# Optimization experiments

Measured on AMD Instinct MI355X. Metric: run time of the kernel, lower is better.

## Reference

```python
import jax, jax.numpy as jnp
import numpy as np

N_NODES = 100000
N_EDGES = 1600000
D_IN = 128
D_HID = 128


def setup_inputs() -> dict:
    key = jax.random.key(0)
    ks = jax.random.split(key, 7)
    s_in = 1.0 / np.sqrt(D_IN)
    s_hid = 1.0 / np.sqrt(D_HID)
    return {
        "x": jax.random.normal(ks[0], (N_NODES, D_IN), dtype=jnp.float32),
        "edge_index": jax.random.randint(ks[1], (2, N_EDGES), 0, N_NODES, dtype=jnp.int64),
        "W1_l": jax.random.normal(ks[2], (D_IN, D_HID), dtype=jnp.float32) * s_in,
        "b1": jnp.zeros((D_HID,), dtype=jnp.float32),
        "W1_r": jax.random.normal(ks[3], (D_IN, D_HID), dtype=jnp.float32) * s_in,
        "W2_l": jax.random.normal(ks[4], (D_HID, D_HID), dtype=jnp.float32) * s_hid,
        "b2": jnp.zeros((D_HID,), dtype=jnp.float32),
        "W2_r": jax.random.normal(ks[5], (D_HID, D_HID), dtype=jnp.float32) * s_hid,
    }


def _mean_aggregate(x, src, dst, num_nodes):
    # messages x[src] mean-aggregated at dst (PyG SAGEConv default aggr='mean')
    msg = jnp.take(x, src, axis=0)                       # [E, D] gather
    summed = jax.ops.segment_sum(msg, dst, num_segments=num_nodes)  # [N, D]
    deg = jax.ops.segment_sum(jnp.ones((src.shape[0],), x.dtype), dst,
                              num_segments=num_nodes)
    return summed / jnp.maximum(deg, 1.0)[:, None]


def _sage_conv(x, src, dst, W_l, b, W_r):
    agg = _mean_aggregate(x, src, dst, x.shape[0])
    # out = lin_l(aggregated neighbors) + lin_r(root)
    return agg @ W_l + b + x @ W_r


def reference(x, edge_index, W1_l, b1, W1_r, W2_l, b2, W2_r):
    src, dst = edge_index[0], edge_index[1]
    h = _sage_conv(x, src, dst, W1_l, b1, W1_r)
    h = jax.nn.relu(h)  # dropout inactive in eval mode
    out = _sage_conv(h, src, dst, W2_l, b2, W2_r)
    return out
```

## Files before the change

kernel.cpp:

```cpp
#include <hip/hip_runtime.h>

#define NN 100000
#define NE 1600000
#define DF 128
#define NBUCK 391
#define PA_BLOCKS 784
#define PB_BLOCKS 391
#define CX_BLOCKS 3125
#define CW_BLOCKS 64
#define AGG_GRID 3128

typedef short short8 __attribute__((ext_vector_type(8)));
typedef float floatx4 __attribute__((ext_vector_type(4)));
typedef float floatx2 __attribute__((ext_vector_type(2)));
typedef unsigned int uintx4 __attribute__((ext_vector_type(4)));
typedef unsigned int uint;
typedef unsigned short ushort;
typedef unsigned char uchar;

static __device__ __forceinline__ ushort f2bf(float f) {
    uint u = __builtin_bit_cast(uint, f);
    return (ushort)((u + 0x7fffu + ((u >> 16) & 1u)) >> 16);
}

__global__ __launch_bounds__(256) void pA_hist(const int* __restrict__ dst,
                                               int* __restrict__ hist,
                                               ushort* __restrict__ rank8) {
    __shared__ int h[NBUCK];
    int tid = threadIdx.x;
    for (int i = tid; i < NBUCK; i += 256) h[i] = 0;
    __syncthreads();
    int eb = blockIdx.x * 2048 + tid;
    #pragma unroll
    for (int k = 0; k < 8; ++k) {
        int e = eb + k * 256;
        if (e < NE) {
            int r = atomicAdd(&h[dst[e] >> 8], 1);
            rank8[e] = (ushort)r;
        }
    }
    __syncthreads();
    int* hrow = hist + blockIdx.x * NBUCK;
    for (int i = tid; i < NBUCK; i += 256) hrow[i] = h[i];
}

__global__ __launch_bounds__(256) void pS2_colscan(int* __restrict__ hist,
                                                   int* __restrict__ gt) {
    __shared__ int ps[256];
    int b = blockIdx.x;
    int tid = threadIdx.x;
    int v[4];
    int sum = 0;
    #pragma unroll
    for (int k = 0; k < 4; ++k) {
        int blk = tid * 4 + k;
        v[k] = (blk < PA_BLOCKS) ? hist[blk * NBUCK + b] : 0;
        sum += v[k];
    }
    ps[tid] = sum;
    __syncthreads();
    for (int st = 1; st < 256; st <<= 1) {
        int t = (tid >= st) ? ps[tid - st] : 0;
        __syncthreads();
        ps[tid] += t;
        __syncthreads();
    }
    int excl = ps[tid] - sum;
    #pragma unroll
    for (int k = 0; k < 4; ++k) {
        int blk = tid * 4 + k;
        if (blk < PA_BLOCKS) hist[blk * NBUCK + b] = excl;
        excl += v[k];
    }
    if (tid == 255) gt[b] = excl;
}

__global__ __launch_bounds__(512) void pS_scan(const int* __restrict__ gt,
                                               int* __restrict__ goff) {
    __shared__ int s[512];
    int tid = threadIdx.x;
    int v = (tid < NBUCK) ? gt[tid] : 0;
    s[tid] = v;
    __syncthreads();
    for (int st = 1; st < 512; st <<= 1) {
        int t = (tid >= st) ? s[tid - st] : 0;
        __syncthreads();
        s[tid] += t;
        __syncthreads();
    }
    if (tid < NBUCK) goff[tid] = s[tid] - v;
    if (tid == 0) goff[NBUCK] = NE;
}

__global__ __launch_bounds__(512) void fused_mid(
        const int* __restrict__ src, const int* __restrict__ dst,
        const ushort* __restrict__ rank8, const int* __restrict__ rel,
        const int* __restrict__ goff, uint2* __restrict__ pairs,
        const float* __restrict__ x, ushort* __restrict__ xb, uint* __restrict__ xf8,
        const float* __restrict__ W1l, const float* __restrict__ W1r,
        const float* __restrict__ W2l, const float* __restrict__ W2r,
        ushort* __restrict__ WT1, ushort* __restrict__ WT2) {
    int bid = blockIdx.x;
    int tid = threadIdx.x;
    if (bid < PB_BLOCKS) {
        int eb = bid * 4096 + tid;
        #pragma unroll
        for (int k = 0; k < 8; ++k) {
            int e = eb + k * 512;
            if (e < NE) {
                int s = src[e];
                int d = dst[e];
                int b = d >> 8;
                int pos = goff[b] + rel[(e >> 11) * NBUCK + b] + (int)rank8[e];
                pairs[pos] = make_uint2((uint)s, (uint)d);
            }
        }
    } else if (bid < PB_BLOCKS + CX_BLOCKS) {
        int j = (bid - PB_BLOCKS) * 512 + tid;
        const float4* xr = (const float4*)x + (size_t)j * 2;
        float4 v0 = xr[0], v1 = xr[1];
        uint4 ob;
        ob.x = (uint)f2bf(v0.x) | ((uint)f2bf(v0.y) << 16);
        ob.y = (uint)f2bf(v0.z) | ((uint)f2bf(v0.w) << 16);
        ob.z = (uint)f2bf(v1.x) | ((uint)f2bf(v1.y) << 16);
        ob.w = (uint)f2bf(v1.z) | ((uint)f2bf(v1.w) << 16);
        ((uint4*)xb)[j] = ob;
        uint pk0 = (uint)__builtin_amdgcn_cvt_pk_fp8_f32(v0.x, v0.y, 0, false);
        pk0 = (uint)__builtin_amdgcn_cvt_pk_fp8_f32(v0.z, v0.w, (int)pk0, true);
        uint pk1 = (uint)__builtin_amdgcn_cvt_pk_fp8_f32(v1.x, v1.y, 0, false);
        pk1 = (uint)__builtin_amdgcn_cvt_pk_fp8_f32(v1.z, v1.w, (int)pk1, true);
        ((uint2*)xf8)[j] = make_uint2(pk0, pk1);
    } else {
        int id = (bid - PB_BLOCKS - CX_BLOCKS) * 512 + tid;
        int n = id >> 8, k = id & 255;
        float a = (k < 128) ? W1l[k * 128 + n] : W1r[(k - 128) * 128 + n];
        float b = (k < 128) ? W2l[k * 128 + n] : W2r[(k - 128) * 128 + n];
        WT1[id] = f2bf(a);
        WT2[id] = f2bf(b);
    }
}

__global__ __launch_bounds__(256) void pC_scatter(const uint2* __restrict__ pairs,
                                                  const int* __restrict__ goff,
                                                  int* __restrict__ off,
                                                  int* __restrict__ srt) {
    __shared__ int deg[256];
    __shared__ int loc[256];
    int b = blockIdx.x;
    int beg = goff[b], end = goff[b + 1];
    int tid = threadIdx.x;
    deg[tid] = 0;
    __syncthreads();
    for (int i = beg + tid; i < end; i += 256)
        atomicAdd(&deg[pairs[i].y & 255], 1);
    __syncthreads();
    int v = deg[tid];
    loc[tid] = v;
    __syncthreads();
    for (int st = 1; st < 256; st <<= 1) {
        int t = (tid >= st) ? loc[tid - st] : 0;
        __syncthreads();
        loc[tid] += t;
        __syncthreads();
    }
    int excl = loc[tid] - v + beg;
    int n = (b << 8) + tid;
    if (n < NN) off[n] = excl;
    __syncthreads();
    deg[tid] = excl;
    __syncthreads();
    for (int i = beg + tid; i < end; i += 256) {
        uint2 pr = pairs[i];
        int pos = atomicAdd(&deg[pr.y & 255], 1);
        srt[pos] = (int)pr.x;
    }
}

static __device__ __forceinline__ void acc16(floatx2* ac, uint4 v) {
    ac[0] += __builtin_amdgcn_cvt_pk_f32_fp8((int)v.x, false);
    ac[1] += __builtin_amdgcn_cvt_pk_f32_fp8((int)v.x, true);
    ac[2] += __builtin_amdgcn_cvt_pk_f32_fp8((int)v.y, false);
    ac[3] += __builtin_amdgcn_cvt_pk_f32_fp8((int)v.y, true);
    ac[4] += __builtin_amdgcn_cvt_pk_f32_fp8((int)v.z, false);
    ac[5] += __builtin_amdgcn_cvt_pk_f32_fp8((int)v.z, true);
    ac[6] += __builtin_amdgcn_cvt_pk_f32_fp8((int)v.w, false);
    ac[7] += __builtin_amdgcn_cvt_pk_f32_fp8((int)v.w, true);
}

#define AGG_LOOP(IDX)                                            \
    {                                                            \
        int i = lb;                                              \
        for (; i + 8 <= le; i += 8) {                            \
            int idx[8];                                          \
            _Pragma("unroll")                                    \
            for (int k = 0; k < 8; ++k) idx[k] = IDX(i + k);     \
            uint4 v[8];                                          \
            _Pragma("unroll")                                    \
            for (int k = 0; k < 8; ++k) v[k] = f[(size_t)idx[k] * 8]; \
            _Pragma("unroll")                                    \
            for (int k = 0; k < 8; ++k) acc16(ac, v[k]);         \
        }                                                        \
        if (i + 4 <= le) {                                       \
            int idx[4];                                          \
            _Pragma("unroll")                                    \
            for (int k = 0; k < 4; ++k) idx[k] = IDX(i + k);     \
            uint4 v[4];                                          \
            _Pragma("unroll")                                    \
            for (int k = 0; k < 4; ++k) v[k] = f[(size_t)idx[k] * 8]; \
            _Pragma("unroll")                                    \
            for (int k = 0; k < 4; ++k) acc16(ac, v[k]);         \
            i += 4;                                              \
        }                                                        \
        for (; i < le; ++i) {                                    \
            uint4 v = f[(size_t)IDX(i) * 8];                     \
            acc16(ac, v);                                        \
        }                                                        \
    }

__global__ __launch_bounds__(256) void agg_csr(const uint* __restrict__ feat8,
                                               const int* __restrict__ srt,
                                               const int* __restrict__ off,
                                               ushort* __restrict__ aggb) {
    __shared__ int sidx[2048];
    int nb = blockIdx.x * 32;
    if (nb >= NN) return;
    int tid = threadIdx.x;

    int segb = off[nb];
    int nend = nb + 32;
    int sege = (nend < NN) ? off[nend] : NE;
    int stage = min(sege - segb, 2048);
    for (int i = tid; i < stage; i += 256) sidx[i] = srt[segb + i];
    __syncthreads();

    int n = nb + (tid >> 3);
    int l = tid & 7;
    if (n >= NN) return;
    const uint4* f = (const uint4*)feat8 + l;

    int beg = off[n];
    int end = (n < NN - 1) ? off[n + 1] : NE;
    int lb = beg - segb, le = end - segb;

    floatx2 ac[8];
    #pragma unroll
    for (int t = 0; t < 8; ++t) ac[t] = (floatx2){0.f, 0.f};

    if (le <= stage) {
        #define IDX_LDS(ii) sidx[ii]
        AGG_LOOP(IDX_LDS)
        #undef IDX_LDS
    } else {
        #define IDX_GBL(ii) srt[segb + (ii)]
        AGG_LOOP(IDX_GBL)
        #undef IDX_GBL
    }

    float inv = 1.0f / fmaxf((float)(end - beg), 1.0f);
    uintx4 o0, o1;
    o0.x = (uint)f2bf(ac[0].x * inv) | ((uint)f2bf(ac[0].y * inv) << 16);
    o0.y = (uint)f2bf(ac[1].x * inv) | ((uint)f2bf(ac[1].y * inv) << 16);
    o0.z = (uint)f2bf(ac[2].x * inv) | ((uint)f2bf(ac[2].y * inv) << 16);
    o0.w = (uint)f2bf(ac[3].x * inv) | ((uint)f2bf(ac[3].y * inv) << 16);
    o1.x = (uint)f2bf(ac[4].x * inv) | ((uint)f2bf(ac[4].y * inv) << 16);
    o1.y = (uint)f2bf(ac[5].x * inv) | ((uint)f2bf(ac[5].y * inv) << 16);
    o1.z = (uint)f2bf(ac[6].x * inv) | ((uint)f2bf(ac[6].y * inv) << 16);
    o1.w = (uint)f2bf(ac[7].x * inv) | ((uint)f2bf(ac[7].y * inv) << 16);
    uintx4* dp = (uintx4*)(aggb + (size_t)n * 128 + l * 16);
    __builtin_nontemporal_store(o0, dp);
    __builtin_nontemporal_store(o1, dp + 1);
}

template <int RELU, int BF16OUT, int F8OUT>
__global__ __launch_bounds__(512, 4) void gemm_mfma(
        const ushort* __restrict__ aggb, const ushort* __restrict__ selfb,
        const ushort* __restrict__ WT, const float* __restrict__ bias,
        void* __restrict__ outv, uchar* __restrict__ f8out) {
    __shared__ ushort sWT[128 * 256];
    const int tid = threadIdx.x;
    const int blk = blockIdx.x;

    #pragma unroll
    for (int it = 0; it < 8; ++it) {
        int flat = it * 512 + tid;
        int col = flat >> 5;
        int c = flat & 31;
        uint4 v = *(const uint4*)(WT + (size_t)col * 256 + c * 8);
        *(uint4*)&sWT[col * 256 + (c ^ (col & 7)) * 8] = v;
    }

    const int w = tid >> 6;
    const int lane = tid & 63;
    const int m = lane & 15;
    const int q = lane >> 4;

    int node_m = blk * 128 + w * 16 + m;
    int cn = node_m < NN ? node_m : NN - 1;
    const ushort* arow = aggb + (size_t)cn * 128;
    const ushort* xrow = selfb + (size_t)cn * 128;
    short8 a[8];
    #pragma unroll
    for (int kk = 0; kk < 4; ++kk) {
        a[kk]     = *(const short8*)(arow + kk * 32 + q * 8);
        a[4 + kk] = *(const short8*)(xrow + kk * 32 + q * 8);
    }

    __syncthreads();

    floatx4 acc[8];
    #pragma unroll
    for (int t = 0; t < 8; ++t) acc[t] = (floatx4){0.f, 0.f, 0.f, 0.f};

    const int m7 = m & 7;
    #pragma unroll
    for (int kk = 0; kk < 8; ++kk) {
        int cx = (kk * 4 + q) ^ m7;
        #pragma unroll
        for (int t = 0; t < 8; ++t) {
            short8 b = *(const short8*)&sWT[(t * 16 + m) * 256 + cx * 8];
            acc[t] = __builtin_amdgcn_mfma_f32_16x16x32_bf16(a[kk], b, acc[t], 0, 0, 0);
        }
    }

    const int node_base = blk * 128 + w * 16 + q * 4;
    #pragma unroll
    for (int t = 0; t < 8; ++t) {
        int col = t * 16 + m;
        float bj = bias[col];
        #pragma unroll
        for (int r = 0; r < 4; ++r) {
            int node = node_base + r;
            if (node < NN) {
                float v = acc[t][r] + bj;
                if (RELU) v = fmaxf(v, 0.0f);
                if (BF16OUT)
                    ((ushort*)outv)[(size_t)node * 128 + col] = f2bf(v);
                else
                    ((float*)outv)[(size_t)node * 128 + col] = v;
                if (F8OUT) {
                    uint pk = (uint)__builtin_amdgcn_cvt_pk_fp8_f32(v, v, 0, false);
                    f8out[(size_t)node * 128 + col] = (uchar)pk;
                }
            }
        }
    }
}

extern "C" void kernel_launch(void* const* d_in, const int* in_sizes, int n_in,
                              void* d_out, int out_size, void* d_ws, size_t ws_size,
                              hipStream_t stream) {
    const float* x   = (const float*)d_in[0];
    const int*   ei  = (const int*)d_in[1];
    const float* W1l = (const float*)d_in[2];
    const float* b1  = (const float*)d_in[3];
    const float* W1r = (const float*)d_in[4];
    const float* W2l = (const float*)d_in[5];
    const float* b2  = (const float*)d_in[6];
    const float* W2r = (const float*)d_in[7];
    float*       out = (float*)d_out;

    const int* src = ei;
    const int* dst = ei + NE;

    char* ws = (char*)d_ws;
    int*    off  = (int*)(ws);
    int*    srt  = (int*)(ws + 400000);
    ushort* WT1  = (ushort*)(ws + 7200000);
    ushort* WT2  = (ushort*)(ws + 7265536);
    ushort* xb   = (ushort*)(ws + 7331072);
    uint*   xf8  = (uint*)(ws + 32931072);
    ushort* aggb = (ushort*)(ws + 45731072);
    ushort* hb   = (ushort*)(ws + 71331072);
    uchar*  hf8  = (uchar*)xf8;
    uint2*  pairs = (uint2*)aggb;
    int*    hist  = (int*)((char*)aggb + 12800000);
    ushort* rank8 = (ushort*)((char*)aggb + 14100000);
    int*    gt    = (int*)((char*)aggb + 17300000);
    int*    goff  = (int*)((char*)aggb + 17302000);

    pA_hist<<<PA_BLOCKS, 256, 0, stream>>>(dst, hist, rank8);
    pS2_colscan<<<NBUCK, 256, 0, stream>>>(hist, gt);
    pS_scan<<<1, 512, 0, stream>>>(gt, goff);
    fused_mid<<<PB_BLOCKS + CX_BLOCKS + CW_BLOCKS, 512, 0, stream>>>(
        src, dst, rank8, hist, goff, pairs, x, xb, xf8,
        W1l, W1r, W2l, W2r, WT1, WT2);
    pC_scatter<<<NBUCK, 256, 0, stream>>>(pairs, goff, off, srt);

    const int gemm_grid = (NN + 127) / 128;

    agg_csr<<<AGG_GRID, 256, 0, stream>>>(xf8, srt, off, aggb);
    gemm_mfma<1, 1, 1><<<gemm_grid, 512, 0, stream>>>(aggb, xb, WT1, b1, hb, hf8);

    agg_csr<<<AGG_GRID, 256, 0, stream>>>((const uint*)hf8, srt, off, aggb);
    gemm_mfma<0, 0, 0><<<gemm_grid, 512, 0, stream>>>(aggb, hb, WT2, b2, out, nullptr);
}
```

Measured before the change: 183.7 us.

## Pack edge pairs into 32-bit words and coarsen histogram/partition blocks

```diff
diff --git a/kernel.cpp b/kernel.cpp
--- a/kernel.cpp
+++ b/kernel.cpp
@@ -4,8 +4,8 @@
 #define NE 1600000
 #define DF 128
 #define NBUCK 391
-#define PA_BLOCKS 784
-#define PB_BLOCKS 391
+#define PA_BLOCKS 196
+#define PB_BLOCKS 196
 #define CX_BLOCKS 3125
 #define CW_BLOCKS 64
 #define AGG_GRID 3128
@@ -14,6 +14,7 @@
 typedef float floatx4 __attribute__((ext_vector_type(4)));
 typedef float floatx2 __attribute__((ext_vector_type(2)));
 typedef unsigned int uintx4 __attribute__((ext_vector_type(4)));
+typedef unsigned int uintx2 __attribute__((ext_vector_type(2)));
 typedef unsigned int uint;
 typedef unsigned short ushort;
 typedef unsigned char uchar;
@@ -30,9 +31,9 @@
     int tid = threadIdx.x;
     for (int i = tid; i < NBUCK; i += 256) h[i] = 0;
     __syncthreads();
-    int eb = blockIdx.x * 2048 + tid;
-    #pragma unroll
-    for (int k = 0; k < 8; ++k) {
+    int eb = blockIdx.x * 8192 + tid;
+    #pragma unroll
+    for (int k = 0; k < 32; ++k) {
         int e = eb + k * 256;
         if (e < NE) {
             int r = atomicAdd(&h[dst[e] >> 8], 1);
@@ -49,15 +50,8 @@
     __shared__ int ps[256];
     int b = blockIdx.x;
     int tid = threadIdx.x;
-    int v[4];
-    int sum = 0;
-    #pragma unroll
-    for (int k = 0; k < 4; ++k) {
-        int blk = tid * 4 + k;
-        v[k] = (blk < PA_BLOCKS) ? hist[blk * NBUCK + b] : 0;
-        sum += v[k];
-    }
-    ps[tid] = sum;
+    int v = (tid < PA_BLOCKS) ? hist[tid * NBUCK + b] : 0;
+    ps[tid] = v;
     __syncthreads();
     for (int st = 1; st < 256; st <<= 1) {
         int t = (tid >= st) ? ps[tid - st] : 0;
@@ -65,14 +59,8 @@
         ps[tid] += t;
         __syncthreads();
     }
-    int excl = ps[tid] - sum;
-    #pragma unroll
-    for (int k = 0; k < 4; ++k) {
-        int blk = tid * 4 + k;
-        if (blk < PA_BLOCKS) hist[blk * NBUCK + b] = excl;
-        excl += v[k];
-    }
-    if (tid == 255) gt[b] = excl;
+    if (tid < PA_BLOCKS) hist[tid * NBUCK + b] = ps[tid] - v;
+    if (tid == 255) gt[b] = ps[255];
 }
 
 __global__ __launch_bounds__(512) void pS_scan(const int* __restrict__ gt,
@@ -95,41 +83,46 @@
 __global__ __launch_bounds__(512) void fused_mid(
         const int* __restrict__ src, const int* __restrict__ dst,
         const ushort* __restrict__ rank8, const int* __restrict__ rel,
-        const int* __restrict__ goff, uint2* __restrict__ pairs,
+        const int* __restrict__ goff, uint* __restrict__ pairs,
         const float* __restrict__ x, ushort* __restrict__ xb, uint* __restrict__ xf8,
         const float* __restrict__ W1l, const float* __restrict__ W1r,
         const float* __restrict__ W2l, const float* __restrict__ W2r,
         ushort* __restrict__ WT1, ushort* __restrict__ WT2) {
+    __shared__ int lbase[NBUCK];
     int bid = blockIdx.x;
     int tid = threadIdx.x;
     if (bid < PB_BLOCKS) {
-        int eb = bid * 4096 + tid;
+        const int* rel_row = rel + bid * NBUCK;
+        for (int i = tid; i < NBUCK; i += 512) lbase[i] = goff[i] + rel_row[i];
+        __syncthreads();
+        int eb = bid * 8192 + tid;
         #pragma unroll
-        for (int k = 0; k < 8; ++k) {
+        for (int k = 0; k < 16; ++k) {
             int e = eb + k * 512;
             if (e < NE) {
                 int s = src[e];
                 int d = dst[e];
                 int b = d >> 8;
-                int pos = goff[b] + rel[(e >> 11) * NBUCK + b] + (int)rank8[e];
-                pairs[pos] = make_uint2((uint)s, (uint)d);
+                int pos = lbase[b] + (int)rank8[e];
+                pairs[pos] = ((uint)(d & 255) << 17) | (uint)s;
             }
         }
     } else if (bid < PB_BLOCKS + CX_BLOCKS) {
         int j = (bid - PB_BLOCKS) * 512 + tid;
         const float4* xr = (const float4*)x + (size_t)j * 2;
         float4 v0 = xr[0], v1 = xr[1];
-        uint4 ob;
+        uintx4 ob;
         ob.x = (uint)f2bf(v0.x) | ((uint)f2bf(v0.y) << 16);
         ob.y = (uint)f2bf(v0.z) | ((uint)f2bf(v0.w) << 16);
         ob.z = (uint)f2bf(v1.x) | ((uint)f2bf(v1.y) << 16);
         ob.w = (uint)f2bf(v1.z) | ((uint)f2bf(v1.w) << 16);
-        ((uint4*)xb)[j] = ob;
+        __builtin_nontemporal_store(ob, (uintx4*)xb + j);
         uint pk0 = (uint)__builtin_amdgcn_cvt_pk_fp8_f32(v0.x, v0.y, 0, false);
         pk0 = (uint)__builtin_amdgcn_cvt_pk_fp8_f32(v0.z, v0.w, (int)pk0, true);
         uint pk1 = (uint)__builtin_amdgcn_cvt_pk_fp8_f32(v1.x, v1.y, 0, false);
         pk1 = (uint)__builtin_amdgcn_cvt_pk_fp8_f32(v1.z, v1.w, (int)pk1, true);
-        ((uint2*)xf8)[j] = make_uint2(pk0, pk1);
+        uintx2 pkv = {pk0, pk1};
+        __builtin_nontemporal_store(pkv, (uintx2*)xf8 + j);
     } else {
         int id = (bid - PB_BLOCKS - CX_BLOCKS) * 512 + tid;
         int n = id >> 8, k = id & 255;
@@ -140,7 +133,7 @@
     }
 }
 
-__global__ __launch_bounds__(256) void pC_scatter(const uint2* __restrict__ pairs,
+__global__ __launch_bounds__(256) void pC_scatter(const uint* __restrict__ pairs,
                                                   const int* __restrict__ goff,
                                                   int* __restrict__ off,
                                                   int* __restrict__ srt) {
@@ -152,7 +145,7 @@
     deg[tid] = 0;
     __syncthreads();
     for (int i = beg + tid; i < end; i += 256)
-        atomicAdd(&deg[pairs[i].y & 255], 1);
+        atomicAdd(&deg[pairs[i] >> 17], 1);
     __syncthreads();
     int v = deg[tid];
     loc[tid] = v;
@@ -170,9 +163,9 @@
     deg[tid] = excl;
     __syncthreads();
     for (int i = beg + tid; i < end; i += 256) {
-        uint2 pr = pairs[i];
-        int pos = atomicAdd(&deg[pr.y & 255], 1);
-        srt[pos] = (int)pr.x;
+        uint pr = pairs[i];
+        int pos = atomicAdd(&deg[pr >> 17], 1);
+        srt[pos] = (int)(pr & 0x1FFFFu);
     }
 }
 
@@ -372,11 +365,11 @@
     ushort* aggb = (ushort*)(ws + 45731072);
     ushort* hb   = (ushort*)(ws + 71331072);
     uchar*  hf8  = (uchar*)xf8;
-    uint2*  pairs = (uint2*)aggb;
-    int*    hist  = (int*)((char*)aggb + 12800000);
-    ushort* rank8 = (ushort*)((char*)aggb + 14100000);
-    int*    gt    = (int*)((char*)aggb + 17300000);
-    int*    goff  = (int*)((char*)aggb + 17302000);
+    uint*   pairs = (uint*)aggb;
+    int*    hist  = (int*)((char*)aggb + 6400000);
+    ushort* rank8 = (ushort*)((char*)aggb + 6720000);
+    int*    gt    = (int*)((char*)aggb + 9920512);
+    int*    goff  = (int*)((char*)aggb + 9922304);
 
     pA_hist<<<PA_BLOCKS, 256, 0, stream>>>(dst, hist, rank8);
     pS2_colscan<<<NBUCK, 256, 0, stream>>>(hist, gt);
```

After: 181.8 us. Within noise of the previous version (-1.0%).
